# Kernel optimization log

Measured on AMD Instinct MI355X. Metric: run time of the kernel, lower is better.

## Reference

```python
import jax, jax.numpy as jnp
import numpy as np
import math

B, N, FEAT, H, NONGT, M, POS = 16, 1024, 768, 8, 20, 10, 64
DG = FEAT // H  # per-head dim = 96
NEG = -9e15


def setup_inputs() -> dict:
    key = jax.random.key(0)
    ks = jax.random.split(key, 14)
    s = 0.02
    return dict(
        roi_feat=jax.random.normal(ks[0], (B, N, FEAT), jnp.float32),
        adj_matrix=jax.random.randint(ks[1], (B, N, NONGT), 0, 2).astype(jnp.int32),
        position_embedding=jax.random.uniform(ks[2], (B, N, NONGT, POS), jnp.float32),
        label_biases_att=jax.random.normal(ks[3], (B, N, NONGT), jnp.float32) * 0.1,
        aux_feat=jax.random.normal(ks[4], (B, 1, FEAT), jnp.float32),
        Wq=jax.random.normal(ks[5], (FEAT, FEAT), jnp.float32) * s,
        bq=jnp.zeros((FEAT,), jnp.float32),
        Wk=jax.random.normal(ks[6], (FEAT, FEAT), jnp.float32) * s,
        bk=jnp.zeros((FEAT,), jnp.float32),
        Wpos=jax.random.normal(ks[7], (POS, H), jnp.float32) * s,
        bpos=jnp.zeros((H,), jnp.float32),
        m_k=jax.random.normal(ks[8], (1, M, FEAT), jnp.float32) * (1.0 / FEAT / H),
        m_v=jax.random.normal(ks[9], (1, M, FEAT), jnp.float32) * (1.0 / M),
        Wout=jax.random.normal(ks[10], (H, DG, FEAT), jnp.float32) * s,  # grouped 1x1 conv: per-head [DG, FEAT]
        bout=jnp.zeros((FEAT,), jnp.float32),
    )


def reference(roi_feat, adj_matrix, position_embedding, label_biases_att, aux_feat,
              Wq, bq, Wk, bk, Wpos, bpos, m_k, m_v, Wout, bout):
    b, n, f = roi_feat.shape
    nongt = min(NONGT, n)
    nongt_feat = roi_feat[:, :nongt]                               # [B,nongt,F]

    q = (roi_feat @ Wq + bq).reshape(b, n, H, DG)                  # [B,N,H,DG]
    scale_m = math.sqrt(f / H)
    mk = scale_m * m_k * aux_feat                                  # [B,M,F] (broadcast)
    mv = scale_m * m_v * aux_feat                                  # [B,M,F]
    k = jnp.concatenate([nongt_feat @ Wk + bk, mk], axis=1)        # [B,K,F], K=nongt+M
    v = jnp.concatenate([nongt_feat, mv], axis=1)                  # [B,K,F]
    kk = k.reshape(b, nongt + M, H, DG)

    # scaled QK^T -> [B,N,H,K]
    aff = jnp.einsum('bnhd,bkhd->bnhk', q, kk) / math.sqrt(DG)

    # geometric position bias: log(max(relu(fc(pos)), 1e-6)) on first nongt keys
    pos = jax.nn.relu(position_embedding @ Wpos + bpos)            # [B,N,nongt,H]
    bias = jnp.log(jnp.maximum(pos, 1e-6))
    aff_n = aff[:, :, :, :nongt] + jnp.transpose(bias, (0, 1, 3, 2))

    # adjacency mask + label bias on first nongt keys
    mask = (adj_matrix > 0)[:, :, None, :]                         # [B,N,1,nongt]
    aff_n = jnp.where(mask, aff_n, NEG) + label_biases_att[:, :, None, :]

    weighted = jnp.concatenate([aff_n, aff[:, :, :, nongt:]], axis=-1)
    p = jax.nn.softmax(weighted, axis=-1)                          # [B,N,H,K]

    out_t = jnp.einsum('bnhk,bkf->bnhf', p, v)                     # [B,N,H,F]
    # weight-normed grouped 1x1 conv == per-head linear F -> DG, concat over heads
    out = jnp.einsum('bnhf,hgf->bnhg', out_t, Wout).reshape(b, n, f) + bout
    return out
```

## Files before the change

### kernel.cpp

```cpp
#include <hip/hip_runtime.h>
#include <hip/hip_bf16.h>
#include <cstdint>

typedef __bf16 bf16;
typedef __bf16 bf16x4 __attribute__((ext_vector_type(4)));
typedef __bf16 bf16x8 __attribute__((ext_vector_type(8)));
typedef float f32x4 __attribute__((ext_vector_type(4)));

#define B_ 16
#define N_ 1024
#define FEAT_ 768
#define H_ 8
#define NONGT_ 20
#define M_ 10
#define POS_ 64
#define DG_ 96
#define KTOT_ 30
#define KPAD_ 32
#define ROWS_ (B_*N_)
#define SCALE_M 9.797958971132712f
#define INV_SQRT_DG 0.10206207261596575f
#define NEG_ -9.0e15f

__device__ __forceinline__ void gload16(const void* g, void* lds) {
  __builtin_amdgcn_global_load_lds(
      (const __attribute__((address_space(1))) unsigned int*)g,
      (__attribute__((address_space(3))) unsigned int*)lds, 16, 0, 0);
}

__device__ __forceinline__ bf16x8 cvt8(float4 a, float4 b) {
  bf16x8 o;
  o[0]=(bf16)a.x; o[1]=(bf16)a.y; o[2]=(bf16)a.z; o[3]=(bf16)a.w;
  o[4]=(bf16)b.x; o[5]=(bf16)b.y; o[6]=(bf16)b.z; o[7]=(bf16)b.w;
  return o;
}

__global__ void prep_kernel(const float* __restrict__ Wq, const float* __restrict__ Wk,
                            const float* __restrict__ Wout, const float* __restrict__ roi,
                            const float* __restrict__ aux, const float* __restrict__ m_v,
                            const float* __restrict__ m_k,
                            bf16* __restrict__ Wq_t, bf16* __restrict__ Wk_t,
                            bf16* __restrict__ Whi, bf16* __restrict__ Wlo,
                            bf16* __restrict__ Vbf, bf16* __restrict__ kbuf)
{
  int idx = blockIdx.x * blockDim.x + threadIdx.x;
  int stride = gridDim.x * blockDim.x;
  for (int i = idx; i < FEAT_*FEAT_; i += stride) {
    int k = i / FEAT_, n = i % FEAT_;
    bf16 q = (bf16)Wq[i], kk = (bf16)Wk[i];
    Wq_t[(size_t)n*FEAT_ + k] = q;
    Wk_t[(size_t)n*FEAT_ + k] = kk;
    float w = Wout[i];
    bf16 hi = (bf16)w;
    Whi[i] = hi;
    Wlo[i] = (bf16)(w - (float)hi);
  }
  for (int i = idx; i < B_*KPAD_*FEAT_; i += stride) {
    int f = i % FEAT_;
    int r = (i / FEAT_) % KPAD_;
    int b = i / (FEAT_*KPAD_);
    float v;
    if (r < NONGT_)      v = roi[((size_t)b*N_ + r)*FEAT_ + f];
    else if (r < KTOT_)  v = SCALE_M * m_v[(r-NONGT_)*FEAT_ + f] * aux[b*FEAT_ + f];
    else                 v = 0.f;
    Vbf[i] = (bf16)v;
  }
  for (int i = idx; i < B_*12*FEAT_; i += stride) {
    int f = i % FEAT_;
    int rr = (i / FEAT_) % 12;
    int b = i / (FEAT_*12);
    float v = (rr < M_) ? SCALE_M * m_k[rr*FEAT_ + f] * aux[b*FEAT_ + f] : 0.f;
    kbuf[((size_t)b*KPAD_ + NONGT_ + rr)*FEAT_ + f] = (bf16)v;
  }
}

__global__ __launch_bounds__(256, 2) void gemm_fused_kernel(
    const float* __restrict__ roi, const bf16* __restrict__ Wq_t,
    const float* __restrict__ bq, bf16* __restrict__ qbuf,
    const bf16* __restrict__ Wk_t, const bf16* __restrict__ Vbf,
    const bf16* __restrict__ Whi, const bf16* __restrict__ Wlo,
    const float* __restrict__ bk, bf16* __restrict__ kbuf,
    bf16* __restrict__ vwT_hi, bf16* __restrict__ vwT_lo)
{
  __shared__ __align__(16) bf16 sA[2*128*32];
  __shared__ __align__(16) bf16 sB[2*128*32];
  const int tid = threadIdx.x;
  const int w = tid >> 6, l = tid & 63;
  const int bx = blockIdx.x;
  const int fr = l & 15, fq = l >> 4, fko = fq << 3;

  if (bx < 768) {
    const int x = bx & 7, j = bx >> 3;
    const int mbase = (x + 8*(j/6)) * 128;
    const int nbase = (j % 6) * 128;
    const int wr = w >> 1, wc = w & 1;
    const int srow = tid >> 2;
    const int scol = (tid & 3) << 3;
    const float* Ag0 = roi + (size_t)(mbase + srow)*FEAT_ + scol;
    const float* Ag1 = Ag0 + (size_t)64*FEAT_;
    const bf16*  Bg0 = Wq_t + (size_t)(nbase + srow)*FEAT_ + scol;
    const bf16*  Bg1 = Bg0 + (size_t)64*FEAT_;
    f32x4 acc[4][4] = {};
    {
      float4 a00 = *(const float4*)Ag0, a01 = *(const float4*)(Ag0 + 4);
      float4 a10 = *(const float4*)Ag1, a11 = *(const float4*)(Ag1 + 4);
      gload16(Bg0, sB + w*512);
      gload16(Bg1, sB + 2048 + w*512);
      *(bf16x8*)(sA + srow*32 + scol) = cvt8(a00, a01);
      *(bf16x8*)(sA + (64 + srow)*32 + scol) = cvt8(a10, a11);
      __syncthreads();
    }
    for (int kt = 0; kt < 24; ++kt) {
      const int cur = (kt & 1) << 12;
      const int nxt = ((kt + 1) & 1) << 12;
      float4 p00, p01, p10, p11;
      if (kt < 23) {
        const float* An0 = Ag0 + (kt + 1)*32;
        const float* An1 = Ag1 + (kt + 1)*32;
        p00 = *(const float4*)An0; p01 = *(const float4*)(An0 + 4);
        p10 = *(const float4*)An1; p11 = *(const float4*)(An1 + 4);
        gload16(Bg0 + (kt + 1)*32, sB + nxt + w*512);
        gload16(Bg1 + (kt + 1)*32, sB + nxt + 2048 + w*512);
      }
      bf16x8 af[4], bff[4];
      #pragma unroll
      for (int m = 0; m < 4; ++m)
        af[m] = *(const bf16x8*)(sA + cur + (wr*64 + m*16 + fr)*32 + fko);
      #pragma unroll
      for (int n = 0; n < 4; ++n)
        bff[n] = *(const bf16x8*)(sB + cur + (wc*64 + n*16 + fr)*32 + fko);
      #pragma unroll
      for (int m = 0; m < 4; ++m) {
        #pragma unroll
        for (int n = 0; n < 4; ++n)
          acc[m][n] = __builtin_amdgcn_mfma_f32_16x16x32_bf16(af[m], bff[n], acc[m][n], 0, 0, 0);
      }
      if (kt < 23) {
        *(bf16x8*)(sA + nxt + srow*32 + scol) = cvt8(p00, p01);
        *(bf16x8*)(sA + nxt + (64 + srow)*32 + scol) = cvt8(p10, p11);
      }
      __syncthreads();
    }
    #pragma unroll
    for (int n = 0; n < 4; ++n) {
      const int col = nbase + wc*64 + n*16 + fr;
      const float bv = bq[col];
      #pragma unroll
      for (int m = 0; m < 4; ++m) {
        const int row = mbase + wr*64 + m*16 + fq*4;
        #pragma unroll
        for (int r = 0; r < 4; ++r)
          qbuf[(size_t)(row + r)*FEAT_ + col] = (bf16)(acc[m][n][r] + bv);
      }
    }
  } else {
    const int widx = (bx - 768)*4 + w;
    const int cbase = (widx % 48) * 16;
    const int by = widx / 48;
    f32x4 acc = {};
    if (by < 32) {
      const float* Ap = roi + ((size_t)(by >> 1)*N_ + (by & 1)*16 + fr)*FEAT_ + fko;
      const bf16* Bp = Wk_t + (size_t)(cbase + fr)*FEAT_ + fko;
      #pragma unroll
      for (int kt = 0; kt < FEAT_/32; ++kt) {
        float4 a0 = *(const float4*)(Ap + kt*32);
        float4 a1 = *(const float4*)(Ap + kt*32 + 4);
        bf16x8 b = *(const bf16x8*)(Bp + kt*32);
        acc = __builtin_amdgcn_mfma_f32_16x16x32_bf16(cvt8(a0, a1), b, acc, 0, 0, 0);
      }
      const float bv = bk[cbase + fr];
      #pragma unroll
      for (int r = 0; r < 4; ++r) {
        const int rl = (by & 1)*16 + fq*4 + r;
        if (rl < NONGT_)
          kbuf[((size_t)(by >> 1)*KPAD_ + rl)*FEAT_ + cbase + fr] = (bf16)(acc[r] + bv);
      }
    } else {
      const int rt = by - 32;
      const bf16* Ap = Vbf + ((size_t)rt*16 + fr)*FEAT_ + fko;
      const bf16* B1 = Whi + (size_t)(cbase + fr)*FEAT_ + fko;
      const bf16* B2 = Wlo + (size_t)(cbase + fr)*FEAT_ + fko;
      f32x4 acc2 = {};
      #pragma unroll
      for (int kt = 0; kt < FEAT_/32; ++kt) {
        bf16x8 a = *(const bf16x8*)(Ap + kt*32);
        acc  = __builtin_amdgcn_mfma_f32_16x16x32_bf16(a, *(const bf16x8*)(B1 + kt*32), acc,  0, 0, 0);
        acc2 = __builtin_amdgcn_mfma_f32_16x16x32_bf16(a, *(const bf16x8*)(B2 + kt*32), acc2, 0, 0, 0);
      }
      #pragma unroll
      for (int r = 0; r < 4; ++r) {
        const int grow = rt*16 + fq*4 + r;
        const int b = grow >> 5, key = grow & 31;
        float vv = acc[r] + acc2[r];
        bf16 vh = (bf16)vv;
        size_t addr = ((size_t)b*FEAT_ + cbase + fr)*KPAD_ + key;
        vwT_hi[addr] = vh;
        vwT_lo[addr] = (bf16)(vv - (float)vh);
      }
    }
  }
}

__global__ __launch_bounds__(64, 4) void posbias_kernel(
    const float* __restrict__ pe, const float* __restrict__ Wpos,
    const float* __restrict__ bpos, float* __restrict__ posb)
{
  __shared__ __align__(16) float spe[NONGT_*68];
  __shared__ __align__(16) float swpT[H_*68];
  __shared__ float sbp[H_];
  const int row = blockIdx.x;
  const int l = threadIdx.x;
  const float* per = pe + (size_t)row*NONGT_*POS_;
  for (int i = l; i < NONGT_*POS_; i += 64) spe[(i >> 6)*68 + (i & 63)] = per[i];
  for (int i = l; i < POS_*H_; i += 64) swpT[(i & 7)*68 + (i >> 3)] = Wpos[i];
  if (l < H_) sbp[l] = bpos[l];
  __syncthreads();
  #pragma unroll
  for (int t = 0; t < 3; ++t) {
    int idx = t*64 + l;
    if (idx < NONGT_*H_) {
      int j = idx >> 3, h = idx & 7;
      float s = sbp[h];
      const float4* a4 = (const float4*)(spe + j*68);
      const float4* b4 = (const float4*)(swpT + h*68);
      #pragma unroll
      for (int p4 = 0; p4 < 16; ++p4) {
        float4 a = a4[p4], bv = b4[p4];
        s += a.x*bv.x + a.y*bv.y + a.z*bv.z + a.w*bv.w;
      }
      s = fmaxf(s, 0.f);
      posb[(size_t)row*160 + h*20 + j] = __logf(fmaxf(s, 1e-6f));
    }
  }
}

__global__ __launch_bounds__(256, 4) void attn_kernel(
    const bf16* __restrict__ qbuf, const bf16* __restrict__ kbuf,
    const bf16* __restrict__ vwT_hi, const bf16* __restrict__ vwT_lo,
    const float* __restrict__ posb, const int* __restrict__ adj,
    const float* __restrict__ lb, const float* __restrict__ bout,
    float* __restrict__ out)
{
  __shared__ __align__(16) bf16 sph[H_*16*40];
  __shared__ __align__(16) bf16 spl[H_*16*40];
  const int tid = threadIdx.x;
  const int w = tid >> 6, l = tid & 63;
  const int fr = l & 15, fq = l >> 4, fko = fq << 3;
  const int row0 = blockIdx.x * 16;
  const int b = blockIdx.y;
  const size_t rabs = (size_t)b*N_ + row0 + fr;

  #pragma unroll
  for (int hi2 = 0; hi2 < 2; ++hi2) {
    const int h = w*2 + hi2;
    const bf16* kp = kbuf + (size_t)b*KPAD_*FEAT_ + h*DG_ + fko;
    const bf16* qp = qbuf + rabs*FEAT_ + h*DG_ + fko;
    f32x4 acc0 = {}, acc1 = {};
    #pragma unroll
    for (int kt = 0; kt < 3; ++kt) {
      bf16x8 qa = *(const bf16x8*)(qp + kt*32);
      bf16x8 k0 = *(const bf16x8*)(kp + (size_t)fr*FEAT_ + kt*32);
      bf16x8 k1 = *(const bf16x8*)(kp + (size_t)(16 + fr)*FEAT_ + kt*32);
      acc0 = __builtin_amdgcn_mfma_f32_16x16x32_bf16(k0, qa, acc0, 0, 0, 0);
      acc1 = __builtin_amdgcn_mfma_f32_16x16x32_bf16(k1, qa, acc1, 0, 0, 0);
    }
    const float* pbr = posb + rabs*160 + h*20;
    const int*   adjr = adj + rabs*20;
    const float* lbr  = lb  + rabs*20;
    float lg[2][4];
    #pragma unroll
    for (int r = 0; r < 4; ++r) {
      int j0 = fq*4 + r;
      float v0 = acc0[r] * INV_SQRT_DG;
      v0 = (adjr[j0] > 0 ? v0 + pbr[j0] : NEG_) + lbr[j0];
      lg[0][r] = v0;
      int j1 = 16 + fq*4 + r;
      float v1 = acc1[r] * INV_SQRT_DG;
      if (j1 < NONGT_)      v1 = (adjr[j1] > 0 ? v1 + pbr[j1] : NEG_) + lbr[j1];
      else if (j1 >= KTOT_) v1 = -3.0e38f;
      lg[1][r] = v1;
    }
    float m = lg[0][0];
    #pragma unroll
    for (int jt = 0; jt < 2; ++jt)
      #pragma unroll
      for (int r = 0; r < 4; ++r) m = fmaxf(m, lg[jt][r]);
    m = fmaxf(m, __shfl_xor(m, 16));
    m = fmaxf(m, __shfl_xor(m, 32));
    float s = 0.f;
    float e[2][4];
    #pragma unroll
    for (int jt = 0; jt < 2; ++jt)
      #pragma unroll
      for (int r = 0; r < 4; ++r) { e[jt][r] = __expf(lg[jt][r] - m); s += e[jt][r]; }
    s += __shfl_xor(s, 16);
    s += __shfl_xor(s, 32);
    const float inv = 1.f / s;
    #pragma unroll
    for (int jt = 0; jt < 2; ++jt) {
      bf16x4 ph, pl;
      #pragma unroll
      for (int r = 0; r < 4; ++r) {
        float p = e[jt][r] * inv;
        ph[r] = (bf16)p;
        pl[r] = (bf16)(p - (float)ph[r]);
      }
      const int off = (h*16 + fr)*40 + jt*16 + fq*4;
      *(bf16x4*)(sph + off) = ph;
      *(bf16x4*)(spl + off) = pl;
    }
    bf16x8 pa_h = *(const bf16x8*)(sph + (h*16 + fr)*40 + fko);
    bf16x8 pa_l = *(const bf16x8*)(spl + (h*16 + fr)*40 + fko);
    #pragma unroll
    for (int ct = 0; ct < 6; ++ct) {
      const int col = h*DG_ + ct*16 + fr;
      const size_t vaddr = ((size_t)b*FEAT_ + col)*KPAD_ + fko;
      bf16x8 vh = *(const bf16x8*)(vwT_hi + vaddr);
      bf16x8 vl = *(const bf16x8*)(vwT_lo + vaddr);
      f32x4 o = {};
      o = __builtin_amdgcn_mfma_f32_16x16x32_bf16(pa_h, vh, o, 0, 0, 0);
      o = __builtin_amdgcn_mfma_f32_16x16x32_bf16(pa_h, vl, o, 0, 0, 0);
      o = __builtin_amdgcn_mfma_f32_16x16x32_bf16(pa_l, vh, o, 0, 0, 0);
      const float bv = bout[col];
      #pragma unroll
      for (int r = 0; r < 4; ++r)
        out[((size_t)b*N_ + row0 + fq*4 + r)*FEAT_ + col] = o[r] + bv;
    }
  }
}

extern "C" void kernel_launch(void* const* d_in, const int* in_sizes, int n_in,
                              void* d_out, int out_size, void* d_ws, size_t ws_size,
                              hipStream_t stream) {
  const float* roi  = (const float*)d_in[0];
  const int*   adj  = (const int*)  d_in[1];
  const float* pe   = (const float*)d_in[2];
  const float* lb   = (const float*)d_in[3];
  const float* aux  = (const float*)d_in[4];
  const float* Wq   = (const float*)d_in[5];
  const float* bq   = (const float*)d_in[6];
  const float* Wk   = (const float*)d_in[7];
  const float* bk   = (const float*)d_in[8];
  const float* Wpos = (const float*)d_in[9];
  const float* bpos = (const float*)d_in[10];
  const float* m_k  = (const float*)d_in[11];
  const float* m_v  = (const float*)d_in[12];
  const float* Wout = (const float*)d_in[13];
  const float* bout = (const float*)d_in[14];
  float* out = (float*)d_out;

  char* pw = (char*)d_ws;
  auto carve = [&](size_t bytes) -> void* {
    void* r = pw; pw += (bytes + 255) & ~(size_t)255; return r;
  };
  bf16*  qbuf   = (bf16*) carve((size_t)ROWS_*FEAT_*2);
  bf16*  Wq_t   = (bf16*) carve((size_t)FEAT_*FEAT_*2);
  bf16*  Wk_t   = (bf16*) carve((size_t)FEAT_*FEAT_*2);
  bf16*  Whi    = (bf16*) carve((size_t)FEAT_*FEAT_*2);
  bf16*  Wlo    = (bf16*) carve((size_t)FEAT_*FEAT_*2);
  bf16*  Vbf    = (bf16*) carve((size_t)B_*KPAD_*FEAT_*2);
  bf16*  kbuf   = (bf16*) carve((size_t)B_*KPAD_*FEAT_*2);
  bf16*  vwT_hi = (bf16*) carve((size_t)B_*FEAT_*KPAD_*2);
  bf16*  vwT_lo = (bf16*) carve((size_t)B_*FEAT_*KPAD_*2);
  float* posb   = (float*)carve((size_t)ROWS_*160*4);

  posbias_kernel<<<dim3(16384), dim3(64), 0, stream>>>(pe, Wpos, bpos, posb);
  prep_kernel<<<dim3(1024), dim3(256), 0, stream>>>(Wq, Wk, Wout, roi, aux, m_v, m_k,
                                                    Wq_t, Wk_t, Whi, Wlo, Vbf, kbuf);
  gemm_fused_kernel<<<dim3(1536), dim3(256), 0, stream>>>(roi, Wq_t, bq, qbuf,
                                                          Wk_t, Vbf, Whi, Wlo, bk, kbuf,
                                                          vwT_hi, vwT_lo);
  attn_kernel<<<dim3(64, 16), dim3(256), 0, stream>>>(qbuf, kbuf, vwT_hi, vwT_lo,
                                                      posb, adj, lb, bout, out);
}
```

Before: 127.6 us.

## Rewrite posbias per-element with double FMA and drop LDS staging in Q GEMM

The position-bias kernel now assigns one (row, key) pair per thread. Each thread reads its 64 position features contiguously, accumulates all 8 heads in double precision, and writes an [j][h]-interleaved layout; the attention kernel indexing is updated to match. The Q projection GEMM drops its LDS double buffering and reads A (converted from fp32) and B directly from global memory into MFMA fragments, with launch bounds raised to 3 blocks per CU. Double-precision FMAs are much slower than fp32 on most hardware. The direct global fragment loads are strided and lose the reuse that LDS staging gave, adding memory traffic in exchange for higher occupancy.

Measured after the change: 192.1 us. +50.6%, slower.

```diff
diff --git a/kernel.cpp b/kernel.cpp
--- a/kernel.cpp
+++ b/kernel.cpp
@@ -21,12 +21,6 @@
 #define SCALE_M 9.797958971132712f
 #define INV_SQRT_DG 0.10206207261596575f
 #define NEG_ -9.0e15f
-
-__device__ __forceinline__ void gload16(const void* g, void* lds) {
-  __builtin_amdgcn_global_load_lds(
-      (const __attribute__((address_space(1))) unsigned int*)g,
-      (__attribute__((address_space(3))) unsigned int*)lds, 16, 0, 0);
-}
 
 __device__ __forceinline__ bf16x8 cvt8(float4 a, float4 b) {
   bf16x8 o;
@@ -74,7 +68,47 @@
   }
 }
 
-__global__ __launch_bounds__(256, 2) void gemm_fused_kernel(
+__global__ __launch_bounds__(256, 8) void posbias_kernel(
+    const float* __restrict__ pe, const float* __restrict__ Wpos,
+    const float* __restrict__ bpos, float* __restrict__ posb)
+{
+  __shared__ __align__(16) float sW[POS_*H_];
+  __shared__ float sbp[H_];
+  const int tid = threadIdx.x;
+  sW[tid] = Wpos[tid];
+  sW[256 + tid] = Wpos[256 + tid];
+  if (tid < H_) sbp[tid] = bpos[tid];
+  __syncthreads();
+  const size_t g = (size_t)blockIdx.x*256 + tid;
+  const float4* per = (const float4*)(pe + g*POS_);
+  double acc[8];
+  #pragma unroll
+  for (int h = 0; h < 8; ++h) acc[h] = (double)sbp[h];
+  #pragma unroll
+  for (int p4 = 0; p4 < 16; ++p4) {
+    float4 a = per[p4];
+    float av[4] = {a.x, a.y, a.z, a.w};
+    #pragma unroll
+    for (int e = 0; e < 4; ++e) {
+      const double ad = (double)av[e];
+      const float* wp = sW + (p4*4 + e)*8;
+      #pragma unroll
+      for (int h = 0; h < 8; ++h)
+        acc[h] = fma(ad, (double)wp[h], acc[h]);
+    }
+  }
+  float o[8];
+  #pragma unroll
+  for (int h = 0; h < 8; ++h) {
+    float x = (float)acc[h];
+    o[h] = __logf(fmaxf(fmaxf(x, 0.f), 1e-6f));
+  }
+  float4* po = (float4*)(posb + g*8);
+  po[0] = (float4){o[0], o[1], o[2], o[3]};
+  po[1] = (float4){o[4], o[5], o[6], o[7]};
+}
+
+__global__ __launch_bounds__(256, 3) void gemm_fused_kernel(
     const float* __restrict__ roi, const bf16* __restrict__ Wq_t,
     const float* __restrict__ bq, bf16* __restrict__ qbuf,
     const bf16* __restrict__ Wk_t, const bf16* __restrict__ Vbf,
@@ -82,8 +116,6 @@
     const float* __restrict__ bk, bf16* __restrict__ kbuf,
     bf16* __restrict__ vwT_hi, bf16* __restrict__ vwT_lo)
 {
-  __shared__ __align__(16) bf16 sA[2*128*32];
-  __shared__ __align__(16) bf16 sB[2*128*32];
   const int tid = threadIdx.x;
   const int w = tid >> 6, l = tid & 63;
   const int bx = blockIdx.x;
@@ -94,52 +126,26 @@
     const int mbase = (x + 8*(j/6)) * 128;
     const int nbase = (j % 6) * 128;
     const int wr = w >> 1, wc = w & 1;
-    const int srow = tid >> 2;
-    const int scol = (tid & 3) << 3;
-    const float* Ag0 = roi + (size_t)(mbase + srow)*FEAT_ + scol;
-    const float* Ag1 = Ag0 + (size_t)64*FEAT_;
-    const bf16*  Bg0 = Wq_t + (size_t)(nbase + srow)*FEAT_ + scol;
-    const bf16*  Bg1 = Bg0 + (size_t)64*FEAT_;
+    const float* Abase = roi  + (size_t)(mbase + wr*64 + fr)*FEAT_ + fko;
+    const bf16*  Bbase = Wq_t + (size_t)(nbase + wc*64 + fr)*FEAT_ + fko;
     f32x4 acc[4][4] = {};
-    {
-      float4 a00 = *(const float4*)Ag0, a01 = *(const float4*)(Ag0 + 4);
-      float4 a10 = *(const float4*)Ag1, a11 = *(const float4*)(Ag1 + 4);
-      gload16(Bg0, sB + w*512);
-      gload16(Bg1, sB + 2048 + w*512);
-      *(bf16x8*)(sA + srow*32 + scol) = cvt8(a00, a01);
-      *(bf16x8*)(sA + (64 + srow)*32 + scol) = cvt8(a10, a11);
-      __syncthreads();
-    }
+    #pragma unroll 2
     for (int kt = 0; kt < 24; ++kt) {
-      const int cur = (kt & 1) << 12;
-      const int nxt = ((kt + 1) & 1) << 12;
-      float4 p00, p01, p10, p11;
-      if (kt < 23) {
-        const float* An0 = Ag0 + (kt + 1)*32;
-        const float* An1 = Ag1 + (kt + 1)*32;
-        p00 = *(const float4*)An0; p01 = *(const float4*)(An0 + 4);
-        p10 = *(const float4*)An1; p11 = *(const float4*)(An1 + 4);
-        gload16(Bg0 + (kt + 1)*32, sB + nxt + w*512);
-        gload16(Bg1 + (kt + 1)*32, sB + nxt + 2048 + w*512);
-      }
       bf16x8 af[4], bff[4];
       #pragma unroll
-      for (int m = 0; m < 4; ++m)
-        af[m] = *(const bf16x8*)(sA + cur + (wr*64 + m*16 + fr)*32 + fko);
+      for (int m = 0; m < 4; ++m) {
+        const float* ap = Abase + (size_t)m*16*FEAT_ + kt*32;
+        af[m] = cvt8(*(const float4*)ap, *(const float4*)(ap + 4));
+      }
       #pragma unroll
       for (int n = 0; n < 4; ++n)
-        bff[n] = *(const bf16x8*)(sB + cur + (wc*64 + n*16 + fr)*32 + fko);
+        bff[n] = *(const bf16x8*)(Bbase + (size_t)n*16*FEAT_ + kt*32);
       #pragma unroll
       for (int m = 0; m < 4; ++m) {
         #pragma unroll
         for (int n = 0; n < 4; ++n)
           acc[m][n] = __builtin_amdgcn_mfma_f32_16x16x32_bf16(af[m], bff[n], acc[m][n], 0, 0, 0);
       }
-      if (kt < 23) {
-        *(bf16x8*)(sA + nxt + srow*32 + scol) = cvt8(p00, p01);
-        *(bf16x8*)(sA + nxt + (64 + srow)*32 + scol) = cvt8(p10, p11);
-      }
-      __syncthreads();
     }
     #pragma unroll
     for (int n = 0; n < 4; ++n) {
@@ -197,39 +203,6 @@
         vwT_hi[addr] = vh;
         vwT_lo[addr] = (bf16)(vv - (float)vh);
       }
-    }
-  }
-}
-
-__global__ __launch_bounds__(64, 4) void posbias_kernel(
-    const float* __restrict__ pe, const float* __restrict__ Wpos,
-    const float* __restrict__ bpos, float* __restrict__ posb)
-{
-  __shared__ __align__(16) float spe[NONGT_*68];
-  __shared__ __align__(16) float swpT[H_*68];
-  __shared__ float sbp[H_];
-  const int row = blockIdx.x;
-  const int l = threadIdx.x;
-  const float* per = pe + (size_t)row*NONGT_*POS_;
-  for (int i = l; i < NONGT_*POS_; i += 64) spe[(i >> 6)*68 + (i & 63)] = per[i];
-  for (int i = l; i < POS_*H_; i += 64) swpT[(i & 7)*68 + (i >> 3)] = Wpos[i];
-  if (l < H_) sbp[l] = bpos[l];
-  __syncthreads();
-  #pragma unroll
-  for (int t = 0; t < 3; ++t) {
-    int idx = t*64 + l;
-    if (idx < NONGT_*H_) {
-      int j = idx >> 3, h = idx & 7;
-      float s = sbp[h];
-      const float4* a4 = (const float4*)(spe + j*68);
-      const float4* b4 = (const float4*)(swpT + h*68);
-      #pragma unroll
-      for (int p4 = 0; p4 < 16; ++p4) {
-        float4 a = a4[p4], bv = b4[p4];
-        s += a.x*bv.x + a.y*bv.y + a.z*bv.z + a.w*bv.w;
-      }
-      s = fmaxf(s, 0.f);
-      posb[(size_t)row*160 + h*20 + j] = __logf(fmaxf(s, 1e-6f));
     }
   }
 }
@@ -264,7 +237,7 @@
       acc0 = __builtin_amdgcn_mfma_f32_16x16x32_bf16(k0, qa, acc0, 0, 0, 0);
       acc1 = __builtin_amdgcn_mfma_f32_16x16x32_bf16(k1, qa, acc1, 0, 0, 0);
     }
-    const float* pbr = posb + rabs*160 + h*20;
+    const float* pbr = posb + rabs*160;
     const int*   adjr = adj + rabs*20;
     const float* lbr  = lb  + rabs*20;
     float lg[2][4];
@@ -272,11 +245,11 @@
     for (int r = 0; r < 4; ++r) {
       int j0 = fq*4 + r;
       float v0 = acc0[r] * INV_SQRT_DG;
-      v0 = (adjr[j0] > 0 ? v0 + pbr[j0] : NEG_) + lbr[j0];
+      v0 = (adjr[j0] > 0 ? v0 + pbr[j0*8 + h] : NEG_) + lbr[j0];
       lg[0][r] = v0;
       int j1 = 16 + fq*4 + r;
       float v1 = acc1[r] * INV_SQRT_DG;
-      if (j1 < NONGT_)      v1 = (adjr[j1] > 0 ? v1 + pbr[j1] : NEG_) + lbr[j1];
+      if (j1 < NONGT_)      v1 = (adjr[j1] > 0 ? v1 + pbr[j1*8 + h] : NEG_) + lbr[j1];
       else if (j1 >= KTOT_) v1 = -3.0e38f;
       lg[1][r] = v1;
     }
@@ -364,7 +337,7 @@
   bf16*  vwT_lo = (bf16*) carve((size_t)B_*FEAT_*KPAD_*2);
   float* posb   = (float*)carve((size_t)ROWS_*160*4);
 
-  posbias_kernel<<<dim3(16384), dim3(64), 0, stream>>>(pe, Wpos, bpos, posb);
+  posbias_kernel<<<dim3(ROWS_*NONGT_/256), dim3(256), 0, stream>>>(pe, Wpos, bpos, posb);
   prep_kernel<<<dim3(1024), dim3(256), 0, stream>>>(Wq, Wk, Wout, roi, aux, m_v, m_k,
                                                     Wq_t, Wk_t, Whi, Wlo, Vbf, kbuf);
   gemm_fused_kernel<<<dim3(1536), dim3(256), 0, stream>>>(roi, Wq_t, bq, qbuf,
```
